# Optimization experiments

Measured on AMD Instinct MI355X. Metric: run time of the kernel, lower is better.

## Reference

```python
import jax, jax.numpy as jnp
import numpy as np
import math

_B, _L, _D, _H = 4, 2048, 512, 8
_DH = _D // _H


def setup_inputs() -> dict:
    key = jax.random.key(0)
    ks = jax.random.split(key, 16)
    w_scale = 1.0 / math.sqrt(_D)
    def lin(kw, kb):
        W = jax.random.uniform(kw, (_D, _D), jnp.float32, -w_scale, w_scale)
        b = jax.random.uniform(kb, (_D,), jnp.float32, -w_scale, w_scale)
        return W, b
    Wq_w, Wq_b = lin(ks[0], ks[1])
    Wk_w, Wk_b = lin(ks[2], ks[3])
    Wv_w, Wv_b = lin(ks[4], ks[5])
    fc_w, fc_b = lin(ks[6], ks[7])
    Q = jax.random.normal(ks[8], (_B, _L, _D), jnp.float32)
    K = jax.random.normal(ks[9], (_B, _L, _D), jnp.float32)
    V = jax.random.normal(ks[10], (_B, _L, _D), jnp.float32)
    # E = torch.rand(L, DH): uniform [0,1), non-trainable buffer
    E = jax.random.uniform(ks[11], (_L, _DH), jnp.float32)
    # causal mask: True (1) where attention is disallowed -> gets -1e9
    mask = jnp.triu(jnp.ones((_L, _L), dtype=bool), k=1)[None, None]  # (1,1,L,L)
    return {"Q": Q, "K": K, "V": V, "mask": mask,
            "Wq_w": Wq_w, "Wq_b": Wq_b, "Wk_w": Wk_w, "Wk_b": Wk_b,
            "Wv_w": Wv_w, "Wv_b": Wv_b, "fc_w": fc_w, "fc_b": fc_b,
            "E": E, "H": _H}


def reference(Q, K, V, mask, Wq_w, Wq_b, Wk_w, Wk_b, Wv_w, Wv_b, fc_w, fc_b, E, H):
    B, Lq, D = Q.shape
    DH = D // H

    def proj(x, W, b):  # torch Linear: x @ W.T + b, then split heads -> (B,H,L,DH)
        y = x @ W.T + b
        return y.reshape(B, -1, H, DH).transpose(0, 2, 1, 3)

    q = proj(Q, Wq_w, Wq_b)
    k = proj(K, Wk_w, Wk_b)
    v = proj(V, Wv_w, Wv_b)
    Lk = k.shape[2]

    # _get_left_embedding: last Lq rows of E
    Eu = E[max(0, E.shape[0] - Lq):, :]            # (e, DH), e == Lq here
    e = Eu.shape[0]

    QE = jnp.einsum('bhld,ed->bhle', q, Eu)        # (B,H,Lq,e)
    # _qe_masking: keep QE[..., i, j] where j >= e-1-i (upper anti-triangle)
    i = jnp.arange(Lq)[:, None]
    j = jnp.arange(e)[None, :]
    keep = (i + j >= e - 1).astype(QE.dtype)
    QE = QE * keep

    # _skewing: pad one zero column, reshape, drop first row
    padded = jnp.pad(QE, ((0, 0), (0, 0), (0, 0), (1, 0)))   # (B,H,Lq,e+1)
    Srel = padded.reshape(B, H, e + 1, Lq)[:, :, 1:, :]      # (B,H,e,Lq)
    if Lk < Lq:
        Srel = Srel[:, :, :, :Lk]

    logits = (jnp.einsum('bhld,bhmd->bhlm', q, k) + Srel) / math.sqrt(DH)
    logits = logits + mask.astype(jnp.float32) * (-1e9)
    AW = jax.nn.softmax(logits, axis=-1)
    out = jnp.einsum('bhlm,bhmd->bhld', AW, v)               # (B,H,Lq,DH)
    out = out.transpose(0, 2, 1, 3).reshape(B, -1, D)        # (B,Lq,D)
    return out @ fc_w.T + fc_b
```

## Files before the change

kernel.cpp:

```cpp
#include <hip/hip_runtime.h>
#include <stdint.h>

typedef __bf16 bf16;
typedef float f32x4 __attribute__((ext_vector_type(4)));
typedef bf16 bf16x8 __attribute__((ext_vector_type(8)));
typedef bf16 bf16x4 __attribute__((ext_vector_type(4)));

#define MFMA16(a, b, c) __builtin_amdgcn_mfma_f32_16x16x32_bf16((a), (b), (c), 0, 0, 0)
#define EXP2F(x) __builtin_amdgcn_exp2f(x)

__device__ __forceinline__ void gll16(const void* g, void* l) {
  __builtin_amdgcn_global_load_lds((const __attribute__((address_space(1))) void*)g,
                                   (__attribute__((address_space(3))) void*)l, 16, 0, 0);
}

__global__ __launch_bounds__(256) void convert_all(
    const float4* __restrict__ Q, const float4* __restrict__ K, const float4* __restrict__ V,
    const float4* __restrict__ Wq, const float4* __restrict__ Wk, const float4* __restrict__ Wv,
    const float4* __restrict__ fcw, const float4* __restrict__ E,
    bf16x4* __restrict__ Xq, bf16x4* __restrict__ Xk, bf16x4* __restrict__ Xv,
    bf16x4* __restrict__ Wqb, bf16x4* __restrict__ Wkb, bf16x4* __restrict__ Wvb,
    bf16x4* __restrict__ fcb, bf16x4* __restrict__ Eb) {
  int i = blockIdx.x * 256 + threadIdx.x;
  const float4* s;
  bf16x4* d;
  int off;
  if (i < 1048576) { s = Q; d = Xq; off = i; }
  else if (i < 2097152) { s = K; d = Xk; off = i - 1048576; }
  else if (i < 3145728) { s = V; d = Xv; off = i - 2097152; }
  else if (i < 3211264) { s = Wq; d = Wqb; off = i - 3145728; }
  else if (i < 3276800) { s = Wk; d = Wkb; off = i - 3211264; }
  else if (i < 3342336) { s = Wv; d = Wvb; off = i - 3276800; }
  else if (i < 3407872) { s = fcw; d = fcb; off = i - 3342336; }
  else { s = E; d = Eb; off = i - 3407872; }
  float4 v = s[off];
  bf16x4 o;
  o[0] = (bf16)v.x; o[1] = (bf16)v.y; o[2] = (bf16)v.z; o[3] = (bf16)v.w;
  d[off] = o;
}

__device__ __forceinline__ void gemm_core(const bf16* __restrict__ A, const bf16* __restrict__ Bt,
                                          bf16* ldsA, bf16* ldsB, int m0, int n0,
                                          f32x4 acc[4][4]) {
  const int t = threadIdx.x;
  const int lane = t & 63, w = t >> 6;
  const int l15 = lane & 15, quad = lane >> 4;
  const int wm = w >> 1, wn = w & 1;
#pragma unroll
  for (int i = 0; i < 4; i++)
#pragma unroll
    for (int j = 0; j < 4; j++) acc[i][j] = (f32x4){0.f, 0.f, 0.f, 0.f};

  const int ch0 = t, ch1 = t + 256;
  const int r0 = ch0 >> 2, c0 = (ch0 & 3) ^ (r0 & 3);
  const int r1 = ch1 >> 2, c1 = (ch1 & 3) ^ (r1 & 3);

  int aoff[4], boff[4];
#pragma unroll
  for (int mt = 0; mt < 4; mt++) {
    int m = wm * 64 + mt * 16 + l15;
    aoff[mt] = (m << 6) + ((quad ^ (l15 & 3)) << 4);
    int n = wn * 64 + mt * 16 + l15;
    boff[mt] = (n << 6) + ((quad ^ (l15 & 3)) << 4);
  }
  bf16* ldsA1 = ldsA + w * 512;
  bf16* ldsA2 = ldsA + 2048 + w * 512;
  bf16* ldsB1 = ldsB + w * 512;
  bf16* ldsB2 = ldsB + 2048 + w * 512;

  for (int kt = 0; kt < 512; kt += 32) {
    gll16(A + (size_t)(m0 + r0) * 512 + kt + c0 * 8, ldsA1);
    gll16(A + (size_t)(m0 + r1) * 512 + kt + c1 * 8, ldsA2);
    gll16(Bt + (size_t)(n0 + r0) * 512 + kt + c0 * 8, ldsB1);
    gll16(Bt + (size_t)(n0 + r1) * 512 + kt + c1 * 8, ldsB2);
    __syncthreads();
    bf16x8 af[4], bfr[4];
#pragma unroll
    for (int mt = 0; mt < 4; mt++) af[mt] = *(const bf16x8*)((const char*)ldsA + aoff[mt]);
#pragma unroll
    for (int nt = 0; nt < 4; nt++) bfr[nt] = *(const bf16x8*)((const char*)ldsB + boff[nt]);
#pragma unroll
    for (int mt = 0; mt < 4; mt++)
#pragma unroll
      for (int nt = 0; nt < 4; nt++)
        acc[mt][nt] = MFMA16(af[mt], bfr[nt], acc[mt][nt]);
    __syncthreads();
  }
}

__global__ __launch_bounds__(256) void proj_gemm(
    const bf16* __restrict__ Xq, const bf16* __restrict__ Xk, const bf16* __restrict__ Xv,
    const bf16* __restrict__ Wq, const bf16* __restrict__ Wk, const bf16* __restrict__ Wv,
    const float* __restrict__ bq, const float* __restrict__ bk, const float* __restrict__ bv,
    bf16* __restrict__ qb, bf16* __restrict__ kb, bf16* __restrict__ vb) {
  __shared__ bf16 ldsA[128 * 32];
  __shared__ bf16 ldsB[128 * 32];
  const int z = blockIdx.z;
  const bf16* A = z == 0 ? Xq : (z == 1 ? Xk : Xv);
  const bf16* W = z == 0 ? Wq : (z == 1 ? Wk : Wv);
  const float* bias = z == 0 ? bq : (z == 1 ? bk : bv);
  bf16* out = z == 0 ? qb : (z == 1 ? kb : vb);
  const int m0 = blockIdx.x * 128, n0 = blockIdx.y * 128;
  f32x4 acc[4][4];
  gemm_core(A, W, ldsA, ldsB, m0, n0, acc);

  const int t = threadIdx.x;
  const int lane = t & 63, w = t >> 6;
  const int l15 = lane & 15, quad = lane >> 4;
  const int wm = w >> 1, wn = w & 1;
#pragma unroll
  for (int mt = 0; mt < 4; mt++)
#pragma unroll
    for (int nt = 0; nt < 4; nt++)
#pragma unroll
      for (int r = 0; r < 4; r++) {
        int gm = m0 + wm * 64 + mt * 16 + quad * 4 + r;
        int gn = n0 + wn * 64 + nt * 16 + l15;
        float v = acc[mt][nt][r] + bias[gn];
        int b = gm >> 11, l = gm & 2047, h = gn >> 6, d = gn & 63;
        out[(((size_t)(b * 8 + h)) * 2048 + l) * 64 + d] = (bf16)v;
      }
}

__global__ __launch_bounds__(256) void final_gemm(const bf16* __restrict__ A,
                                                  const bf16* __restrict__ W,
                                                  const float* __restrict__ bias,
                                                  float* __restrict__ out) {
  __shared__ bf16 ldsA[128 * 32];
  __shared__ bf16 ldsB[128 * 32];
  const int m0 = blockIdx.x * 128, n0 = blockIdx.y * 128;
  f32x4 acc[4][4];
  gemm_core(A, W, ldsA, ldsB, m0, n0, acc);

  const int t = threadIdx.x;
  const int lane = t & 63, w = t >> 6;
  const int l15 = lane & 15, quad = lane >> 4;
  const int wm = w >> 1, wn = w & 1;
#pragma unroll
  for (int mt = 0; mt < 4; mt++)
#pragma unroll
    for (int nt = 0; nt < 4; nt++)
#pragma unroll
      for (int r = 0; r < 4; r++) {
        int gm = m0 + wm * 64 + mt * 16 + quad * 4 + r;
        int gn = n0 + wn * 64 + nt * 16 + l15;
        out[(size_t)gm * 512 + gn] = acc[mt][nt][r] + bias[gn];
      }
}

__global__ __launch_bounds__(256) void transpose_v(const bf16* __restrict__ vbuf,
                                                   bf16* __restrict__ vT) {
  __shared__ bf16 tile[64][72];
  const int bh = blockIdx.y, l0 = blockIdx.x * 64;
  const bf16* src = vbuf + ((size_t)bh * 2048 + l0) * 64;
  bf16* dst = vT + (size_t)bh * 64 * 2048 + l0;
  const int t = threadIdx.x;
#pragma unroll
  for (int p = 0; p < 2; p++) {
    int ch = t + p * 256;
    int r = ch >> 3, c8 = ch & 7;
    *(bf16x8*)&tile[r][c8 * 8] = *(const bf16x8*)&src[(size_t)r * 64 + c8 * 8];
  }
  __syncthreads();
#pragma unroll
  for (int p = 0; p < 2; p++) {
    int ch = t + p * 256;
    int dr = ch >> 3, lc = ch & 7;
    bf16x8 v;
#pragma unroll
    for (int j = 0; j < 8; j++) v[j] = tile[lc * 8 + j][dr];
    *(bf16x8*)&dst[(size_t)dr * 2048 + lc * 8] = v;
  }
}

__global__ __launch_bounds__(256, 3) void attn_kernel(const bf16* __restrict__ qbuf,
                                                      const bf16* __restrict__ kbuf,
                                                      const bf16* __restrict__ vT,
                                                      const bf16* __restrict__ Eb,
                                                      bf16* __restrict__ attn) {
  __shared__ bf16 Kl[2][64 * 64];
  __shared__ bf16 Vl[2][64 * 64];
  __shared__ bf16 Pl[4][16 * 72];
  const int t = threadIdx.x, w = t >> 6, lane = t & 63;
  const int l15 = lane & 15, quad = lane >> 4;
  const int x = blockIdx.x;
  const int pid = x & 511, phase = x >> 9;
  const int a = pid & 15, bh = pid >> 4;
  const int t4 = phase ? a : 31 - a;
  const int i0 = t4 * 64 + w * 16;
  bf16* Pw = Pl[w];
  const bf16* qh = qbuf + (size_t)bh * 2048 * 64;
  const bf16* kh = kbuf + (size_t)bh * 2048 * 64;
  const bf16* vh = vT + (size_t)bh * 64 * 2048;

  const int sr0 = t >> 3, sc0 = (t & 7) ^ (sr0 & 7);
  const int sr1 = sr0 + 32;
  const int b0 = (t & 192) * 16;
  const int b1 = 4096 + b0;

  int bpaddr[4];
  bool loA[4];
#pragma unroll
  for (int r = 0; r < 4; r++) {
    int u = quad * 4 + r;
    bpaddr[r] = (((l15 + 15 - u) & 15) + 16 * quad) * 4;
    loA[r] = (l15 <= u);
  }

  bf16x8 aq0, aq1;
  {
    const bf16* qrow = qh + (size_t)(i0 + l15) * 64 + quad * 8;
    aq0 = *(const bf16x8*)qrow;
    aq1 = *(const bf16x8*)(qrow + 32);
  }
  bf16x8 ones;
#pragma unroll
  for (int j = 0; j < 8; j++) ones[j] = (bf16)1.0f;

  f32x4 O[4], Osum;
  Osum = (f32x4){0.f, 0.f, 0.f, 0.f};
#pragma unroll
  for (int i = 0; i < 4; i++) O[i] = (f32x4){0.f, 0.f, 0.f, 0.f};
  const float sc = 0.125f * 1.44269504088896f;
  const int ebase0 = 2047 - i0 - 15;

  gll16(kh + (size_t)sr0 * 64 + sc0 * 8, (char*)&Kl[0][0] + b0);
  gll16(kh + (size_t)sr1 * 64 + sc0 * 8, (char*)&Kl[0][0] + b1);
  gll16(vh + (size_t)sr0 * 2048 + sc0 * 8, (char*)&Vl[0][0] + b0);
  gll16(vh + (size_t)sr1 * 2048 + sc0 * 8, (char*)&Vl[0][0] + b1);

  float Bpc[4];
  {
    int er = ebase0 + l15;
    er = er > 2047 ? 2047 : er;
    const bf16* erow = Eb + (size_t)er * 64 + quad * 8;
    bf16x8 e0 = *(const bf16x8*)erow;
    bf16x8 e1 = *(const bf16x8*)(erow + 32);
    f32x4 zz = (f32x4){0.f, 0.f, 0.f, 0.f};
    zz = MFMA16(aq0, e0, zz);
    zz = MFMA16(aq1, e1, zz);
#pragma unroll
    for (int r = 0; r < 4; r++)
      Bpc[r] = __int_as_float(__builtin_amdgcn_ds_bpermute(bpaddr[r], __float_as_int(zz[r])));
  }

  for (int jt = 0; jt <= t4; jt++) {
    const int j0 = jt * 64;
    const int cur = jt & 1;
    const bool diag = (jt == t4);
    float Bp[5][4];
#pragma unroll
    for (int r = 0; r < 4; r++) Bp[0][r] = Bpc[r];
    const int ebase = ebase0 + j0;
#pragma unroll
    for (int nt = 1; nt < 5; nt++) {
      int er = ebase + nt * 16 + l15;
      er = er > 2047 ? 2047 : er;
      const bf16* erow = Eb + (size_t)er * 64 + quad * 8;
      bf16x8 e0 = *(const bf16x8*)erow;
      bf16x8 e1 = *(const bf16x8*)(erow + 32);
      f32x4 zz = (f32x4){0.f, 0.f, 0.f, 0.f};
      zz = MFMA16(aq0, e0, zz);
      zz = MFMA16(aq1, e1, zz);
#pragma unroll
      for (int r = 0; r < 4; r++)
        Bp[nt][r] =
            __int_as_float(__builtin_amdgcn_ds_bpermute(bpaddr[r], __float_as_int(zz[r])));
    }
#pragma unroll
    for (int r = 0; r < 4; r++) Bpc[r] = Bp[4][r];

    __syncthreads();
    if (jt < t4) {
      const int nb = cur ^ 1, nj = j0 + 64;
      gll16(kh + (size_t)(nj + sr0) * 64 + sc0 * 8, (char*)&Kl[nb][0] + b0);
      gll16(kh + (size_t)(nj + sr1) * 64 + sc0 * 8, (char*)&Kl[nb][0] + b1);
      gll16(vh + (size_t)sr0 * 2048 + nj + sc0 * 8, (char*)&Vl[nb][0] + b0);
      gll16(vh + (size_t)sr1 * 2048 + nj + sc0 * 8, (char*)&Vl[nb][0] + b1);
    }
    const bf16* Kc = Kl[cur];
    const bf16* Vc = Vl[cur];
    f32x4 s[4];
#pragma unroll
    for (int nt = 0; nt < 4; nt++) {
      int row = nt * 16 + l15;
      bf16x8 k0 = *(const bf16x8*)(Kc + ((row << 3) + (quad ^ (row & 7))) * 8);
      bf16x8 k1 = *(const bf16x8*)(Kc + ((row << 3) + ((quad + 4) ^ (row & 7))) * 8);
      f32x4 zz = (f32x4){0.f, 0.f, 0.f, 0.f};
      zz = MFMA16(aq0, k0, zz);
      s[nt] = MFMA16(aq1, k1, zz);
    }
    if (diag) {
#pragma unroll
      for (int nt = 0; nt < 4; nt++)
#pragma unroll
        for (int r = 0; r < 4; r++) {
          int u = quad * 4 + r;
          int j = nt * 16 + l15;
          float skew = loA[r] ? Bp[nt][r] : Bp[nt + 1][r];
          float logit = (s[nt][r] + skew) * sc;
          if (j0 + j > i0 + u) logit = -1e30f;
          Pw[u * 72 + j] = (bf16)EXP2F(logit);
        }
    } else {
#pragma unroll
      for (int nt = 0; nt < 4; nt++)
#pragma unroll
        for (int r = 0; r < 4; r++) {
          int u = quad * 4 + r;
          int j = nt * 16 + l15;
          float skew = loA[r] ? Bp[nt][r] : Bp[nt + 1][r];
          Pw[u * 72 + j] = (bf16)EXP2F((s[nt][r] + skew) * sc);
        }
    }
    bf16x8 pa0 = *(const bf16x8*)&Pw[l15 * 72 + quad * 8];
    bf16x8 pa1 = *(const bf16x8*)&Pw[l15 * 72 + 32 + quad * 8];
    Osum = MFMA16(pa0, ones, Osum);
    Osum = MFMA16(pa1, ones, Osum);
#pragma unroll
    for (int nt = 0; nt < 4; nt++) {
      int row = nt * 16 + l15;
      bf16x8 v0 = *(const bf16x8*)(Vc + ((row << 3) + (quad ^ (row & 7))) * 8);
      bf16x8 v1 = *(const bf16x8*)(Vc + ((row << 3) + ((quad + 4) ^ (row & 7))) * 8);
      O[nt] = MFMA16(pa0, v0, O[nt]);
      O[nt] = MFMA16(pa1, v1, O[nt]);
    }
  }
  const int b = bh >> 3, hh = bh & 7;
  float inv[4];
#pragma unroll
  for (int r = 0; r < 4; r++) inv[r] = 1.0f / Osum[r];
  bf16* orow = attn + ((size_t)(b * 2048 + i0)) * 512 + hh * 64;
#pragma unroll
  for (int nt = 0; nt < 4; nt++)
#pragma unroll
    for (int r = 0; r < 4; r++)
      orow[(size_t)(quad * 4 + r) * 512 + nt * 16 + l15] = (bf16)(O[nt][r] * inv[r]);
}

extern "C" void kernel_launch(void* const* d_in, const int* in_sizes, int n_in,
                              void* d_out, int out_size, void* d_ws, size_t ws_size,
                              hipStream_t stream) {
  const float* Q = (const float*)d_in[0];
  const float* K = (const float*)d_in[1];
  const float* V = (const float*)d_in[2];
  const float* Wq = (const float*)d_in[4];
  const float* bq = (const float*)d_in[5];
  const float* Wk = (const float*)d_in[6];
  const float* bk = (const float*)d_in[7];
  const float* Wv = (const float*)d_in[8];
  const float* bv = (const float*)d_in[9];
  const float* fcw = (const float*)d_in[10];
  const float* fcb = (const float*)d_in[11];
  const float* E = (const float*)d_in[12];

  char* ws = (char*)d_ws;
  bf16* Xq = (bf16*)(ws + 0);
  bf16* Xk = (bf16*)(ws + 8388608);
  bf16* Xv = (bf16*)(ws + 16777216);
  bf16* Wqb = (bf16*)(ws + 25165824);
  bf16* Wkb = (bf16*)(ws + 25690112);
  bf16* Wvb = (bf16*)(ws + 26214400);
  bf16* fcwb = (bf16*)(ws + 26738688);
  bf16* Eb = (bf16*)(ws + 27262976);
  bf16* qbuf = (bf16*)(ws + 27525120);
  bf16* kbuf = (bf16*)(ws + 35913728);
  bf16* vbuf = (bf16*)(ws + 44302336);
  bf16* vTb = Xk;
  bf16* attnb = Xq;

  convert_all<<<13440, 256, 0, stream>>>(
      (const float4*)Q, (const float4*)K, (const float4*)V, (const float4*)Wq,
      (const float4*)Wk, (const float4*)Wv, (const float4*)fcw, (const float4*)E,
      (bf16x4*)Xq, (bf16x4*)Xk, (bf16x4*)Xv, (bf16x4*)Wqb, (bf16x4*)Wkb,
      (bf16x4*)Wvb, (bf16x4*)fcwb, (bf16x4*)Eb);

  proj_gemm<<<dim3(64, 4, 3), 256, 0, stream>>>(Xq, Xk, Xv, Wqb, Wkb, Wvb, bq, bk, bv,
                                                qbuf, kbuf, vbuf);

  transpose_v<<<dim3(32, 32), 256, 0, stream>>>(vbuf, vTb);

  attn_kernel<<<1024, 256, 0, stream>>>(qbuf, kbuf, vTb, Eb, attnb);

  final_gemm<<<dim3(64, 4, 1), 256, 0, stream>>>(attnb, fcwb, fcb, (float*)d_out);
}
```

Baseline: 250.9 us.

## Split long causal attention strips into two KV halves with separate normalization pass

The attention kernel now splits the work for the upper query strips into two KV ranges, so every block processes at most 16 KV tiles. Partial unnormalized outputs and row sums are written to workspace, and a new norm kernel adds the halves and divides. The K/V shared-memory double buffer is dropped to a single buffer so occupancy can rise from 3 to 4 blocks per CU. The costs are an extra kernel launch, extra global traffic for the partial results, and loads that are no longer overlapped with compute.

```diff
diff --git a/kernel.cpp b/kernel.cpp
--- a/kernel.cpp
+++ b/kernel.cpp
@@ -173,21 +173,28 @@
   }
 }
 
-__global__ __launch_bounds__(256, 3) void attn_kernel(const bf16* __restrict__ qbuf,
-                                                      const bf16* __restrict__ kbuf,
-                                                      const bf16* __restrict__ vT,
-                                                      const bf16* __restrict__ Eb,
-                                                      bf16* __restrict__ attn) {
-  __shared__ bf16 Kl[2][64 * 64];
-  __shared__ bf16 Vl[2][64 * 64];
+__global__ __launch_bounds__(256, 4) void attn_kernel(
+    const bf16* __restrict__ qbuf, const bf16* __restrict__ kbuf,
+    const bf16* __restrict__ vT, const bf16* __restrict__ Eb,
+    bf16* __restrict__ attnb, bf16* __restrict__ Of1,
+    float* __restrict__ Os0, float* __restrict__ Os1) {
+  __shared__ bf16 Kl[64 * 64];
+  __shared__ bf16 Vl[64 * 64];
   __shared__ bf16 Pl[4][16 * 72];
   const int t = threadIdx.x, w = t >> 6, lane = t & 63;
   const int l15 = lane & 15, quad = lane >> 4;
   const int x = blockIdx.x;
-  const int pid = x & 511, phase = x >> 9;
-  const int a = pid & 15, bh = pid >> 4;
-  const int t4 = phase ? a : 31 - a;
-  const int i0 = t4 * 64 + w * 16;
+  const int bh = x & 31, job = x >> 5;
+  int strip, jt0, jt1;
+  bool isB;
+  if (job < 16) {
+    strip = 16 + job; jt0 = 0; jt1 = 16; isB = false;
+  } else {
+    int k = job - 16, i = k >> 1;
+    if ((k & 1) == 0) { strip = 15 - i; jt0 = 0; jt1 = 16 - i; isB = false; }
+    else { strip = 31 - i; jt0 = 16; jt1 = 32 - i; isB = true; }
+  }
+  const int i0 = strip * 64 + w * 16;
   bf16* Pw = Pl[w];
   const bf16* qh = qbuf + (size_t)bh * 2048 * 64;
   const bf16* kh = kbuf + (size_t)bh * 2048 * 64;
@@ -195,8 +202,8 @@
 
   const int sr0 = t >> 3, sc0 = (t & 7) ^ (sr0 & 7);
   const int sr1 = sr0 + 32;
-  const int b0 = (t & 192) * 16;
-  const int b1 = 4096 + b0;
+  const int wb0 = (t & 192) * 16;
+  const int wb1 = 4096 + wb0;
 
   int bpaddr[4];
   bool loA[4];
@@ -222,16 +229,11 @@
 #pragma unroll
   for (int i = 0; i < 4; i++) O[i] = (f32x4){0.f, 0.f, 0.f, 0.f};
   const float sc = 0.125f * 1.44269504088896f;
-  const int ebase0 = 2047 - i0 - 15;
-
-  gll16(kh + (size_t)sr0 * 64 + sc0 * 8, (char*)&Kl[0][0] + b0);
-  gll16(kh + (size_t)sr1 * 64 + sc0 * 8, (char*)&Kl[0][0] + b1);
-  gll16(vh + (size_t)sr0 * 2048 + sc0 * 8, (char*)&Vl[0][0] + b0);
-  gll16(vh + (size_t)sr1 * 2048 + sc0 * 8, (char*)&Vl[0][0] + b1);
+  const int ebase00 = 2047 - i0 - 15;
 
   float Bpc[4];
   {
-    int er = ebase0 + l15;
+    int er = ebase00 + jt0 * 64 + l15;
     er = er > 2047 ? 2047 : er;
     const bf16* erow = Eb + (size_t)er * 64 + quad * 8;
     bf16x8 e0 = *(const bf16x8*)erow;
@@ -244,14 +246,18 @@
       Bpc[r] = __int_as_float(__builtin_amdgcn_ds_bpermute(bpaddr[r], __float_as_int(zz[r])));
   }
 
-  for (int jt = 0; jt <= t4; jt++) {
+  for (int jt = jt0; jt < jt1; jt++) {
     const int j0 = jt * 64;
-    const int cur = jt & 1;
-    const bool diag = (jt == t4);
+    const bool diag = (jt == strip);
+    __syncthreads();
+    gll16(kh + (size_t)(j0 + sr0) * 64 + sc0 * 8, (char*)Kl + wb0);
+    gll16(kh + (size_t)(j0 + sr1) * 64 + sc0 * 8, (char*)Kl + wb1);
+    gll16(vh + (size_t)sr0 * 2048 + j0 + sc0 * 8, (char*)Vl + wb0);
+    gll16(vh + (size_t)sr1 * 2048 + j0 + sc0 * 8, (char*)Vl + wb1);
     float Bp[5][4];
 #pragma unroll
     for (int r = 0; r < 4; r++) Bp[0][r] = Bpc[r];
-    const int ebase = ebase0 + j0;
+    const int ebase = ebase00 + j0;
 #pragma unroll
     for (int nt = 1; nt < 5; nt++) {
       int er = ebase + nt * 16 + l15;
@@ -271,21 +277,12 @@
     for (int r = 0; r < 4; r++) Bpc[r] = Bp[4][r];
 
     __syncthreads();
-    if (jt < t4) {
-      const int nb = cur ^ 1, nj = j0 + 64;
-      gll16(kh + (size_t)(nj + sr0) * 64 + sc0 * 8, (char*)&Kl[nb][0] + b0);
-      gll16(kh + (size_t)(nj + sr1) * 64 + sc0 * 8, (char*)&Kl[nb][0] + b1);
-      gll16(vh + (size_t)sr0 * 2048 + nj + sc0 * 8, (char*)&Vl[nb][0] + b0);
-      gll16(vh + (size_t)sr1 * 2048 + nj + sc0 * 8, (char*)&Vl[nb][0] + b1);
-    }
-    const bf16* Kc = Kl[cur];
-    const bf16* Vc = Vl[cur];
     f32x4 s[4];
 #pragma unroll
     for (int nt = 0; nt < 4; nt++) {
       int row = nt * 16 + l15;
-      bf16x8 k0 = *(const bf16x8*)(Kc + ((row << 3) + (quad ^ (row & 7))) * 8);
-      bf16x8 k1 = *(const bf16x8*)(Kc + ((row << 3) + ((quad + 4) ^ (row & 7))) * 8);
+      bf16x8 k0 = *(const bf16x8*)(Kl + ((row << 3) + (quad ^ (row & 7))) * 8);
+      bf16x8 k1 = *(const bf16x8*)(Kl + ((row << 3) + ((quad + 4) ^ (row & 7))) * 8);
       f32x4 zz = (f32x4){0.f, 0.f, 0.f, 0.f};
       zz = MFMA16(aq0, k0, zz);
       s[nt] = MFMA16(aq1, k1, zz);
@@ -320,22 +317,63 @@
 #pragma unroll
     for (int nt = 0; nt < 4; nt++) {
       int row = nt * 16 + l15;
-      bf16x8 v0 = *(const bf16x8*)(Vc + ((row << 3) + (quad ^ (row & 7))) * 8);
-      bf16x8 v1 = *(const bf16x8*)(Vc + ((row << 3) + ((quad + 4) ^ (row & 7))) * 8);
+      bf16x8 v0 = *(const bf16x8*)(Vl + ((row << 3) + (quad ^ (row & 7))) * 8);
+      bf16x8 v1 = *(const bf16x8*)(Vl + ((row << 3) + ((quad + 4) ^ (row & 7))) * 8);
       O[nt] = MFMA16(pa0, v0, O[nt]);
       O[nt] = MFMA16(pa1, v1, O[nt]);
     }
   }
-  const int b = bh >> 3, hh = bh & 7;
-  float inv[4];
-#pragma unroll
-  for (int r = 0; r < 4; r++) inv[r] = 1.0f / Osum[r];
-  bf16* orow = attn + ((size_t)(b * 2048 + i0)) * 512 + hh * 64;
-#pragma unroll
-  for (int nt = 0; nt < 4; nt++)
-#pragma unroll
-    for (int r = 0; r < 4; r++)
-      orow[(size_t)(quad * 4 + r) * 512 + nt * 16 + l15] = (bf16)(O[nt][r] * inv[r]);
+  if (isB) {
+    bf16* orow = Of1 + ((size_t)(bh * 1024 + (i0 - 1024))) * 64;
+#pragma unroll
+    for (int nt = 0; nt < 4; nt++)
+#pragma unroll
+      for (int r = 0; r < 4; r++)
+        orow[(size_t)(quad * 4 + r) * 64 + nt * 16 + l15] = (bf16)O[nt][r];
+    if (l15 == 0) {
+#pragma unroll
+      for (int r = 0; r < 4; r++) Os1[bh * 1024 + (i0 - 1024) + quad * 4 + r] = Osum[r];
+    }
+  } else {
+    const int b = bh >> 3, hh = bh & 7;
+    bf16* orow = attnb + ((size_t)(b * 2048 + i0)) * 512 + hh * 64;
+#pragma unroll
+    for (int nt = 0; nt < 4; nt++)
+#pragma unroll
+      for (int r = 0; r < 4; r++)
+        orow[(size_t)(quad * 4 + r) * 512 + nt * 16 + l15] = (bf16)O[nt][r];
+    if (l15 == 0) {
+#pragma unroll
+      for (int r = 0; r < 4; r++) Os0[bh * 2048 + i0 + quad * 4 + r] = Osum[r];
+    }
+  }
+}
+
+__global__ __launch_bounds__(256) void norm_kernel(bf16x8* __restrict__ attnb,
+                                                   const bf16x8* __restrict__ Of1,
+                                                   const float* __restrict__ Os0,
+                                                   const float* __restrict__ Os1) {
+  int i = blockIdx.x * 256 + threadIdx.x;
+  int col8 = i & 63;
+  int row = i >> 6;
+  int b = row >> 11, l = row & 2047, h = col8 >> 3;
+  int bh = b * 8 + h;
+  float s = Os0[bh * 2048 + l];
+  bf16x8 v0 = attnb[i];
+  float acc[8];
+#pragma unroll
+  for (int j = 0; j < 8; j++) acc[j] = (float)v0[j];
+  if (l >= 1024) {
+    s += Os1[bh * 1024 + l - 1024];
+    bf16x8 v1 = Of1[(size_t)(bh * 1024 + l - 1024) * 8 + (col8 & 7)];
+#pragma unroll
+    for (int j = 0; j < 8; j++) acc[j] += (float)v1[j];
+  }
+  float inv = 1.0f / s;
+  bf16x8 o;
+#pragma unroll
+  for (int j = 0; j < 8; j++) o[j] = (bf16)(acc[j] * inv);
+  attnb[i] = o;
 }
 
 extern "C" void kernel_launch(void* const* d_in, const int* in_sizes, int n_in,
@@ -366,6 +404,9 @@
   bf16* qbuf = (bf16*)(ws + 27525120);
   bf16* kbuf = (bf16*)(ws + 35913728);
   bf16* vbuf = (bf16*)(ws + 44302336);
+  bf16* Of1 = (bf16*)(ws + 52690944);
+  float* Os0 = (float*)(ws + 56885248);
+  float* Os1 = (float*)(ws + 57147392);
   bf16* vTb = Xk;
   bf16* attnb = Xq;
 
@@ -380,7 +421,9 @@
 
   transpose_v<<<dim3(32, 32), 256, 0, stream>>>(vbuf, vTb);
 
-  attn_kernel<<<1024, 256, 0, stream>>>(qbuf, kbuf, vTb, Eb, attnb);
+  attn_kernel<<<1536, 256, 0, stream>>>(qbuf, kbuf, vTb, Eb, attnb, Of1, Os0, Os1);
+
+  norm_kernel<<<2048, 256, 0, stream>>>((bf16x8*)attnb, (const bf16x8*)Of1, Os0, Os1);
 
   final_gemm<<<dim3(64, 4, 1), 256, 0, stream>>>(attnb, fcwb, fcb, (float*)d_out);
 }
```

Result: no change. 247.3 us (-1.4%).
